# Performance work log

Measured on AMD Instinct MI355X. Metric: run time of the kernel, lower is better.

The kernel has to match this reference:

```python
import jax, jax.numpy as jnp
import numpy as np

N_NODES = 100000
N_EDGES = 3200000
F_IN = 256
F_OUT = 256


def setup_inputs() -> dict:
    key = jax.random.key(0)
    k1, k2, k3, k4, k5, k6 = jax.random.split(key, 6)
    x = jax.random.normal(k1, (N_NODES, F_IN), dtype=jnp.float32)
    edge_rows = jax.random.randint(k2, (N_EDGES,), 0, N_NODES, dtype=jnp.int64)
    edge_cols = jax.random.randint(k3, (N_EDGES,), 0, N_NODES, dtype=jnp.int64)
    edge_vals = jax.random.uniform(k4, (N_EDGES,), dtype=jnp.float32)
    weight = jax.random.normal(k5, (F_IN, F_OUT), dtype=jnp.float32) * (1.0 / np.sqrt(F_OUT))
    b = jax.random.normal(k6, (F_OUT,), dtype=jnp.float32) * (1.0 / np.sqrt(F_OUT))
    return {"x": x, "edge_rows": edge_rows, "edge_cols": edge_cols,
            "edge_vals": edge_vals, "weight": weight, "b": b}


def reference(x, edge_rows, edge_cols, edge_vals, weight, b):
    # support = X @ W  (dense GEMM)
    support = x @ weight  # (N, F_out)
    # SpMM: out[r] = sum_e vals[e] * support[cols[e]] for edges with rows[e]==r
    gathered = edge_vals[:, None] * support[edge_cols]  # (E, F_out)
    out = jax.ops.segment_sum(gathered, edge_rows, num_segments=N_NODES)
    return out + b
```

## Files before the change

### kernel.cpp

```cpp
#include <hip/hip_runtime.h>


#define SH 6
#define BROWS 64
#define CAPSLOT 2560
#define ACHUNK 16384
#define MAXNB 2048

using short8 = __attribute__((ext_vector_type(8))) short;
using f32x4  = __attribute__((ext_vector_type(4))) float;

__device__ __forceinline__ float bf2f(unsigned short h) {
  union { unsigned u; float f; } v; v.u = ((unsigned)h) << 16; return v.f;
}
__device__ __forceinline__ unsigned short f2bf(float f) {
  union { float f; unsigned u; } v; v.f = f;
  unsigned u = v.u;
  unsigned r = (u + 0x7FFFu + ((u >> 16) & 1u)) >> 16;
  return (unsigned short)r;
}

__global__ void k_conv_w(const float* __restrict__ W,
                         unsigned short* __restrict__ Whi,
                         unsigned short* __restrict__ Wlo) {
  int bx = blockIdx.x;
  int lane = threadIdx.x;
  int t = bx >> 3, s = bx & 7;
  int n  = t * 16 + (lane & 15);
  int k0 = s * 32 + (lane >> 4) * 8;
  unsigned short hh[8], ll[8];
#pragma unroll
  for (int j = 0; j < 8; ++j) {
    float w = W[(k0 + j) * 256 + n];
    unsigned short h = f2bf(w);
    hh[j] = h;
    ll[j] = f2bf(w - bf2f(h));
  }
  uint4 uh, ul;
  uh.x = (unsigned)hh[0] | ((unsigned)hh[1] << 16);
  uh.y = (unsigned)hh[2] | ((unsigned)hh[3] << 16);
  uh.z = (unsigned)hh[4] | ((unsigned)hh[5] << 16);
  uh.w = (unsigned)hh[6] | ((unsigned)hh[7] << 16);
  ul.x = (unsigned)ll[0] | ((unsigned)ll[1] << 16);
  ul.y = (unsigned)ll[2] | ((unsigned)ll[3] << 16);
  ul.z = (unsigned)ll[4] | ((unsigned)ll[5] << 16);
  ul.w = (unsigned)ll[6] | ((unsigned)ll[7] << 16);
  size_t o = ((size_t)bx * 64 + lane) * 8;
  *(uint4*)(Whi + o) = uh;
  *(uint4*)(Wlo + o) = ul;
}

__global__ __launch_bounds__(256) void k_gemm(const float* __restrict__ x,
                                              const unsigned short* __restrict__ Whi,
                                              const unsigned short* __restrict__ Wlo,
                                              unsigned short* __restrict__ sup,
                                              int n_nodes) {
  __shared__ alignas(16) unsigned short Ahi[8 * 512];
  __shared__ alignas(16) unsigned short Alo[8 * 512];
  const int m0 = blockIdx.x * 16;
  {
    int t = threadIdx.x;
    int row = t >> 4;
    int kbase = (t & 15) << 4;
    int s = kbase >> 5;
    int quad0 = (kbase >> 3) & 3;
    float v[16];
    int gr = m0 + row;
    if (gr < n_nodes) {
      const float4* px = (const float4*)(x + (size_t)gr * 256 + kbase);
#pragma unroll
      for (int q = 0; q < 4; ++q) {
        float4 f = px[q];
        v[q * 4 + 0] = f.x; v[q * 4 + 1] = f.y; v[q * 4 + 2] = f.z; v[q * 4 + 3] = f.w;
      }
    } else {
#pragma unroll
      for (int j = 0; j < 16; ++j) v[j] = 0.0f;
    }
    unsigned short h[16], l[16];
#pragma unroll
    for (int j = 0; j < 16; ++j) {
      unsigned short hb = f2bf(v[j]);
      h[j] = hb;
      l[j] = f2bf(v[j] - bf2f(hb));
    }
    uint4 u;
    u.x = (unsigned)h[0] | ((unsigned)h[1] << 16);
    u.y = (unsigned)h[2] | ((unsigned)h[3] << 16);
    u.z = (unsigned)h[4] | ((unsigned)h[5] << 16);
    u.w = (unsigned)h[6] | ((unsigned)h[7] << 16);
    *(uint4*)&Ahi[s * 512 + (quad0 * 16 + row) * 8] = u;
    u.x = (unsigned)h[8]  | ((unsigned)h[9]  << 16);
    u.y = (unsigned)h[10] | ((unsigned)h[11] << 16);
    u.z = (unsigned)h[12] | ((unsigned)h[13] << 16);
    u.w = (unsigned)h[14] | ((unsigned)h[15] << 16);
    *(uint4*)&Ahi[s * 512 + ((quad0 + 1) * 16 + row) * 8] = u;
    u.x = (unsigned)l[0] | ((unsigned)l[1] << 16);
    u.y = (unsigned)l[2] | ((unsigned)l[3] << 16);
    u.z = (unsigned)l[4] | ((unsigned)l[5] << 16);
    u.w = (unsigned)l[6] | ((unsigned)l[7] << 16);
    *(uint4*)&Alo[s * 512 + (quad0 * 16 + row) * 8] = u;
    u.x = (unsigned)l[8]  | ((unsigned)l[9]  << 16);
    u.y = (unsigned)l[10] | ((unsigned)l[11] << 16);
    u.z = (unsigned)l[12] | ((unsigned)l[13] << 16);
    u.w = (unsigned)l[14] | ((unsigned)l[15] << 16);
    *(uint4*)&Alo[s * 512 + ((quad0 + 1) * 16 + row) * 8] = u;
  }
  __syncthreads();
  const int lane = threadIdx.x & 63;
  const int wave = threadIdx.x >> 6;
  f32x4 acc0 = {0,0,0,0}, acc1 = {0,0,0,0}, acc2 = {0,0,0,0}, acc3 = {0,0,0,0};
  const short8* AH = (const short8*)Ahi;
  const short8* AL = (const short8*)Alo;
  const short8* BH = (const short8*)Whi;
  const short8* BL = (const short8*)Wlo;
  const int tn = wave * 4;
#pragma unroll
  for (int s = 0; s < 8; ++s) {
    short8 ah = AH[s * 64 + lane];
    short8 al = AL[s * 64 + lane];
    short8 bh0 = BH[((tn + 0) * 8 + s) * 64 + lane];
    short8 bh1 = BH[((tn + 1) * 8 + s) * 64 + lane];
    short8 bh2 = BH[((tn + 2) * 8 + s) * 64 + lane];
    short8 bh3 = BH[((tn + 3) * 8 + s) * 64 + lane];
    short8 bl0 = BL[((tn + 0) * 8 + s) * 64 + lane];
    short8 bl1 = BL[((tn + 1) * 8 + s) * 64 + lane];
    short8 bl2 = BL[((tn + 2) * 8 + s) * 64 + lane];
    short8 bl3 = BL[((tn + 3) * 8 + s) * 64 + lane];
    acc0 = __builtin_amdgcn_mfma_f32_16x16x32_bf16(ah, bh0, acc0, 0, 0, 0);
    acc1 = __builtin_amdgcn_mfma_f32_16x16x32_bf16(ah, bh1, acc1, 0, 0, 0);
    acc2 = __builtin_amdgcn_mfma_f32_16x16x32_bf16(ah, bh2, acc2, 0, 0, 0);
    acc3 = __builtin_amdgcn_mfma_f32_16x16x32_bf16(ah, bh3, acc3, 0, 0, 0);
    acc0 = __builtin_amdgcn_mfma_f32_16x16x32_bf16(ah, bl0, acc0, 0, 0, 0);
    acc1 = __builtin_amdgcn_mfma_f32_16x16x32_bf16(ah, bl1, acc1, 0, 0, 0);
    acc2 = __builtin_amdgcn_mfma_f32_16x16x32_bf16(ah, bl2, acc2, 0, 0, 0);
    acc3 = __builtin_amdgcn_mfma_f32_16x16x32_bf16(ah, bl3, acc3, 0, 0, 0);
    acc0 = __builtin_amdgcn_mfma_f32_16x16x32_bf16(al, bh0, acc0, 0, 0, 0);
    acc1 = __builtin_amdgcn_mfma_f32_16x16x32_bf16(al, bh1, acc1, 0, 0, 0);
    acc2 = __builtin_amdgcn_mfma_f32_16x16x32_bf16(al, bh2, acc2, 0, 0, 0);
    acc3 = __builtin_amdgcn_mfma_f32_16x16x32_bf16(al, bh3, acc3, 0, 0, 0);
  }
  const int quad = lane >> 4;
  const int col  = lane & 15;
  f32x4 accs[4] = {acc0, acc1, acc2, acc3};
#pragma unroll
  for (int i = 0; i < 4; ++i) {
    int n = (tn + i) * 16 + col;
#pragma unroll
    for (int r = 0; r < 4; ++r) {
      int m = m0 + quad * 4 + r;
      if (m < n_nodes) sup[(size_t)m * 256 + n] = f2bf(accs[i][r]);
    }
  }
}

__global__ __launch_bounds__(256) void k_bscatter(const int* __restrict__ rows,
                                                  const int* __restrict__ cols,
                                                  const float* __restrict__ vals,
                                                  unsigned* __restrict__ bucketCount,
                                                  uint2* __restrict__ cvA,
                                                  int E, int NB) {
  __shared__ unsigned h[MAXNB];
  __shared__ unsigned baseS[MAXNB];
  for (int i = threadIdx.x; i < NB; i += 256) h[i] = 0;
  __syncthreads();
  int base = blockIdx.x * ACHUNK;
  int lim = min(ACHUNK, E - base);
  for (int i = threadIdx.x; i < lim; i += 256)
    atomicAdd(&h[rows[base + i] >> SH], 1u);
  __syncthreads();
  for (int i = threadIdx.x; i < NB; i += 256) {
    unsigned c = h[i];
    baseS[i] = c ? ((unsigned)i * CAPSLOT + atomicAdd(&bucketCount[i], c)) : 0u;
  }
  __syncthreads();
  for (int i = threadIdx.x; i < NB; i += 256) h[i] = 0;
  __syncthreads();
  for (int i = threadIdx.x; i < lim; i += 256) {
    int e = base + i;
    int r = rows[e];
    int b = r >> SH;
    unsigned off = atomicAdd(&h[b], 1u);
    unsigned pos = baseS[b] + off;
    union { float f; unsigned u; } v; v.f = vals[e];
    unsigned key = (unsigned)cols[e] | ((unsigned)(r & (BROWS - 1)) << 17);
    cvA[pos] = make_uint2(key, v.u);
  }
}

__global__ __launch_bounds__(256) void k_bspmm(const unsigned* __restrict__ bucketCount,
                                               const uint2* __restrict__ cvA,
                                               const unsigned short* __restrict__ sup,
                                               const float* __restrict__ bias,
                                               float* __restrict__ out,
                                               int n_nodes) {
  __shared__ uint2 scv[CAPSLOT];
  __shared__ unsigned hist[BROWS];
  __shared__ unsigned startS[BROWS + 1];
  __shared__ unsigned cur[BROWS];
  const int b = blockIdx.x;
  const int tid = threadIdx.x;
  const unsigned beg = (unsigned)b * CAPSLOT;
  int cnt = (int)bucketCount[b];
  if (cnt > CAPSLOT) cnt = CAPSLOT;
  if (tid < BROWS) hist[tid] = 0;
  __syncthreads();
  for (int i = tid; i < cnt; i += 256)
    atomicAdd(&hist[cvA[beg + i].x >> 17], 1u);
  __syncthreads();
  if (tid == 0) {
    unsigned run = 0;
#pragma unroll
    for (int j = 0; j < BROWS; ++j) { startS[j] = run; run += hist[j]; }
    startS[BROWS] = run;
  }
  __syncthreads();
  if (tid < BROWS) cur[tid] = startS[tid];
  __syncthreads();
  for (int i = tid; i < cnt; i += 256) {
    uint2 c = cvA[beg + i];
    unsigned p = atomicAdd(&cur[c.x >> 17], 1u);
    scv[p] = c;
  }
  __syncthreads();
  const int wave = tid >> 6;
  const int lane = tid & 63;
  const unsigned short* supl = sup + lane * 4;
  float4 b4 = *(const float4*)(bias + lane * 4);
  for (int lr = wave; lr < BROWS; lr += 4) {
    int gr = (b << SH) + lr;
    if (gr >= n_nodes) break;
    float ax = b4.x, ay = b4.y, az = b4.z, aw = b4.w;
    unsigned e = startS[lr], t1 = startS[lr + 1];
    for (; e + 8 <= t1; e += 8) {
      uint2 c[8]; ushort4 g[8];
#pragma unroll
      for (int j = 0; j < 8; ++j) c[j] = scv[e + j];
#pragma unroll
      for (int j = 0; j < 8; ++j)
        g[j] = *(const ushort4*)(supl + (size_t)(c[j].x & 0x1FFFFu) * 256);
#pragma unroll
      for (int j = 0; j < 8; ++j) {
        union { unsigned u; float f; } v{c[j].y};
        ax = fmaf(v.f, bf2f(g[j].x), ax); ay = fmaf(v.f, bf2f(g[j].y), ay);
        az = fmaf(v.f, bf2f(g[j].z), az); aw = fmaf(v.f, bf2f(g[j].w), aw);
      }
    }
    for (; e + 4 <= t1; e += 4) {
      uint2 c[4]; ushort4 g[4];
#pragma unroll
      for (int j = 0; j < 4; ++j) c[j] = scv[e + j];
#pragma unroll
      for (int j = 0; j < 4; ++j)
        g[j] = *(const ushort4*)(supl + (size_t)(c[j].x & 0x1FFFFu) * 256);
#pragma unroll
      for (int j = 0; j < 4; ++j) {
        union { unsigned u; float f; } v{c[j].y};
        ax = fmaf(v.f, bf2f(g[j].x), ax); ay = fmaf(v.f, bf2f(g[j].y), ay);
        az = fmaf(v.f, bf2f(g[j].z), az); aw = fmaf(v.f, bf2f(g[j].w), aw);
      }
    }
    for (; e < t1; ++e) {
      uint2 c = scv[e];
      ushort4 g = *(const ushort4*)(supl + (size_t)(c.x & 0x1FFFFu) * 256);
      union { unsigned u; float f; } v{c.y};
      ax = fmaf(v.f, bf2f(g.x), ax); ay = fmaf(v.f, bf2f(g.y), ay);
      az = fmaf(v.f, bf2f(g.z), az); aw = fmaf(v.f, bf2f(g.w), aw);
    }
    float4 o; o.x = ax; o.y = ay; o.z = az; o.w = aw;
    *(float4*)(out + (size_t)gr * 256 + lane * 4) = o;
  }
}

extern "C" void kernel_launch(void* const* d_in, const int* in_sizes, int n_in,
                              void* d_out, int out_size, void* d_ws, size_t ws_size,
                              hipStream_t stream) {
  const float* x    = (const float*)d_in[0];
  const int*   rows = (const int*)d_in[1];
  const int*   cols = (const int*)d_in[2];
  const float* vals = (const float*)d_in[3];
  const float* W    = (const float*)d_in[4];
  const float* bias = (const float*)d_in[5];
  float* out = (float*)d_out;

  const int n_nodes = in_sizes[0] / 256;
  const int E       = in_sizes[1];
  const int NB      = (n_nodes + BROWS - 1) >> SH;
  (void)n_in; (void)out_size; (void)ws_size;

  char* ws = (char*)d_ws;
  size_t off = 0;
  auto alloc = [&](size_t bytes) { size_t o = off; off += (bytes + 255) & ~(size_t)255; return o; };
  unsigned short* Whi    = (unsigned short*)(ws + alloc(65536 * 2));
  unsigned short* Wlo    = (unsigned short*)(ws + alloc(65536 * 2));
  unsigned short* sup    = (unsigned short*)(ws + alloc((size_t)n_nodes * 256 * 2));
  unsigned* bucketCount  = (unsigned*)(ws + alloc((size_t)NB * 4));
  uint2* cvA             = (uint2*)(ws + alloc((size_t)NB * CAPSLOT * 8));

  const int nA = (E + ACHUNK - 1) / ACHUNK;

  hipMemsetAsync(bucketCount, 0, (size_t)NB * 4, stream);
  k_conv_w<<<128, 64, 0, stream>>>(W, Whi, Wlo);
  k_gemm<<<(n_nodes + 15) / 16, 256, 0, stream>>>(x, Whi, Wlo, sup, n_nodes);
  k_bscatter<<<nA, 256, 0, stream>>>(rows, cols, vals, bucketCount, cvA, E, NB);
  k_bspmm<<<NB, 256, 0, stream>>>(bucketCount, cvA, sup, bias, out, n_nodes);
}
```

Baseline: 621.7 us.

## Fuse GEMM and edge bucket scatter into one launch, halve bucket size

```diff
diff --git a/kernel.cpp b/kernel.cpp
--- a/kernel.cpp
+++ b/kernel.cpp
@@ -1,11 +1,11 @@
 #include <hip/hip_runtime.h>
 
 
-#define SH 6
-#define BROWS 64
-#define CAPSLOT 2560
-#define ACHUNK 16384
-#define MAXNB 2048
+#define SH 5
+#define BROWS 32
+#define CAPSLOT 1280
+#define ACHUNK 8192
+#define MAXNB 3200
 
 using short8 = __attribute__((ext_vector_type(8))) short;
 using f32x4  = __attribute__((ext_vector_type(4))) float;
@@ -50,14 +50,52 @@
   *(uint4*)(Wlo + o) = ul;
 }
 
-__global__ __launch_bounds__(256) void k_gemm(const float* __restrict__ x,
-                                              const unsigned short* __restrict__ Whi,
-                                              const unsigned short* __restrict__ Wlo,
-                                              unsigned short* __restrict__ sup,
-                                              int n_nodes) {
-  __shared__ alignas(16) unsigned short Ahi[8 * 512];
-  __shared__ alignas(16) unsigned short Alo[8 * 512];
-  const int m0 = blockIdx.x * 16;
+struct GemmSmem { alignas(16) unsigned short Ahi[8 * 512]; alignas(16) unsigned short Alo[8 * 512]; };
+struct ScatSmem { unsigned h[MAXNB]; };
+
+__global__ __launch_bounds__(256) void k_gemm_scatter(
+    const float* __restrict__ x,
+    const unsigned short* __restrict__ Whi,
+    const unsigned short* __restrict__ Wlo,
+    unsigned short* __restrict__ sup,
+    int n_nodes,
+    const int* __restrict__ rows,
+    const int* __restrict__ cols,
+    const float* __restrict__ vals,
+    unsigned* __restrict__ bucketCount,
+    uint2* __restrict__ cvA,
+    int E, int NB, int nScat) {
+  __shared__ union { GemmSmem g; ScatSmem s; } sm;
+
+  if ((int)blockIdx.x < nScat) {
+    unsigned* h = sm.s.h;
+    int base = (int)blockIdx.x * ACHUNK;
+    int lim = min(ACHUNK, E - base);
+    for (int i = threadIdx.x; i < NB; i += 256) h[i] = 0u;
+    __syncthreads();
+    for (int i = threadIdx.x; i < lim; i += 256)
+      atomicAdd(&h[rows[base + i] >> SH], 1u);
+    __syncthreads();
+    for (int i = threadIdx.x; i < NB; i += 256) {
+      unsigned c = h[i];
+      if (c) h[i] = (unsigned)i * CAPSLOT + atomicAdd(&bucketCount[i], c);
+    }
+    __syncthreads();
+    for (int i = threadIdx.x; i < lim; i += 256) {
+      int e = base + i;
+      int r = rows[e];
+      unsigned pos = atomicAdd(&h[r >> SH], 1u);
+      union { float f; unsigned u; } v;
+      v.f = __builtin_nontemporal_load(vals + e);
+      unsigned key = (unsigned)__builtin_nontemporal_load(cols + e) |
+                     ((unsigned)(r & (BROWS - 1)) << 17);
+      unsigned long long pk = (unsigned long long)key | ((unsigned long long)v.u << 32);
+      __builtin_nontemporal_store(pk, (unsigned long long*)&cvA[pos]);
+    }
+    return;
+  }
+
+  const int m0 = ((int)blockIdx.x - nScat) * 16;
   {
     int t = threadIdx.x;
     int row = t >> 4;
@@ -67,11 +105,11 @@
     float v[16];
     int gr = m0 + row;
     if (gr < n_nodes) {
-      const float4* px = (const float4*)(x + (size_t)gr * 256 + kbase);
+      const f32x4* px = (const f32x4*)(x + (size_t)gr * 256 + kbase);
 #pragma unroll
       for (int q = 0; q < 4; ++q) {
-        float4 f = px[q];
-        v[q * 4 + 0] = f.x; v[q * 4 + 1] = f.y; v[q * 4 + 2] = f.z; v[q * 4 + 3] = f.w;
+        f32x4 f = __builtin_nontemporal_load(px + q);
+        v[q * 4 + 0] = f[0]; v[q * 4 + 1] = f[1]; v[q * 4 + 2] = f[2]; v[q * 4 + 3] = f[3];
       }
     } else {
 #pragma unroll
@@ -89,29 +127,29 @@
     u.y = (unsigned)h[2] | ((unsigned)h[3] << 16);
     u.z = (unsigned)h[4] | ((unsigned)h[5] << 16);
     u.w = (unsigned)h[6] | ((unsigned)h[7] << 16);
-    *(uint4*)&Ahi[s * 512 + (quad0 * 16 + row) * 8] = u;
+    *(uint4*)&sm.g.Ahi[s * 512 + (quad0 * 16 + row) * 8] = u;
     u.x = (unsigned)h[8]  | ((unsigned)h[9]  << 16);
     u.y = (unsigned)h[10] | ((unsigned)h[11] << 16);
     u.z = (unsigned)h[12] | ((unsigned)h[13] << 16);
     u.w = (unsigned)h[14] | ((unsigned)h[15] << 16);
-    *(uint4*)&Ahi[s * 512 + ((quad0 + 1) * 16 + row) * 8] = u;
+    *(uint4*)&sm.g.Ahi[s * 512 + ((quad0 + 1) * 16 + row) * 8] = u;
     u.x = (unsigned)l[0] | ((unsigned)l[1] << 16);
     u.y = (unsigned)l[2] | ((unsigned)l[3] << 16);
     u.z = (unsigned)l[4] | ((unsigned)l[5] << 16);
     u.w = (unsigned)l[6] | ((unsigned)l[7] << 16);
-    *(uint4*)&Alo[s * 512 + (quad0 * 16 + row) * 8] = u;
+    *(uint4*)&sm.g.Alo[s * 512 + (quad0 * 16 + row) * 8] = u;
     u.x = (unsigned)l[8]  | ((unsigned)l[9]  << 16);
     u.y = (unsigned)l[10] | ((unsigned)l[11] << 16);
     u.z = (unsigned)l[12] | ((unsigned)l[13] << 16);
     u.w = (unsigned)l[14] | ((unsigned)l[15] << 16);
-    *(uint4*)&Alo[s * 512 + ((quad0 + 1) * 16 + row) * 8] = u;
+    *(uint4*)&sm.g.Alo[s * 512 + ((quad0 + 1) * 16 + row) * 8] = u;
   }
   __syncthreads();
   const int lane = threadIdx.x & 63;
   const int wave = threadIdx.x >> 6;
   f32x4 acc0 = {0,0,0,0}, acc1 = {0,0,0,0}, acc2 = {0,0,0,0}, acc3 = {0,0,0,0};
-  const short8* AH = (const short8*)Ahi;
-  const short8* AL = (const short8*)Alo;
+  const short8* AH = (const short8*)sm.g.Ahi;
+  const short8* AL = (const short8*)sm.g.Alo;
   const short8* BH = (const short8*)Whi;
   const short8* BL = (const short8*)Wlo;
   const int tn = wave * 4;
@@ -154,40 +192,6 @@
   }
 }
 
-__global__ __launch_bounds__(256) void k_bscatter(const int* __restrict__ rows,
-                                                  const int* __restrict__ cols,
-                                                  const float* __restrict__ vals,
-                                                  unsigned* __restrict__ bucketCount,
-                                                  uint2* __restrict__ cvA,
-                                                  int E, int NB) {
-  __shared__ unsigned h[MAXNB];
-  __shared__ unsigned baseS[MAXNB];
-  for (int i = threadIdx.x; i < NB; i += 256) h[i] = 0;
-  __syncthreads();
-  int base = blockIdx.x * ACHUNK;
-  int lim = min(ACHUNK, E - base);
-  for (int i = threadIdx.x; i < lim; i += 256)
-    atomicAdd(&h[rows[base + i] >> SH], 1u);
-  __syncthreads();
-  for (int i = threadIdx.x; i < NB; i += 256) {
-    unsigned c = h[i];
-    baseS[i] = c ? ((unsigned)i * CAPSLOT + atomicAdd(&bucketCount[i], c)) : 0u;
-  }
-  __syncthreads();
-  for (int i = threadIdx.x; i < NB; i += 256) h[i] = 0;
-  __syncthreads();
-  for (int i = threadIdx.x; i < lim; i += 256) {
-    int e = base + i;
-    int r = rows[e];
-    int b = r >> SH;
-    unsigned off = atomicAdd(&h[b], 1u);
-    unsigned pos = baseS[b] + off;
-    union { float f; unsigned u; } v; v.f = vals[e];
-    unsigned key = (unsigned)cols[e] | ((unsigned)(r & (BROWS - 1)) << 17);
-    cvA[pos] = make_uint2(key, v.u);
-  }
-}
-
 __global__ __launch_bounds__(256) void k_bspmm(const unsigned* __restrict__ bucketCount,
                                                const uint2* __restrict__ cvA,
                                                const unsigned short* __restrict__ sup,
@@ -226,11 +230,11 @@
   const int wave = tid >> 6;
   const int lane = tid & 63;
   const unsigned short* supl = sup + lane * 4;
-  float4 b4 = *(const float4*)(bias + lane * 4);
+  f32x4 b4 = *(const f32x4*)(bias + lane * 4);
   for (int lr = wave; lr < BROWS; lr += 4) {
     int gr = (b << SH) + lr;
     if (gr >= n_nodes) break;
-    float ax = b4.x, ay = b4.y, az = b4.z, aw = b4.w;
+    float ax = b4[0], ay = b4[1], az = b4[2], aw = b4[3];
     unsigned e = startS[lr], t1 = startS[lr + 1];
     for (; e + 8 <= t1; e += 8) {
       uint2 c[8]; ushort4 g[8];
@@ -267,8 +271,8 @@
       ax = fmaf(v.f, bf2f(g.x), ax); ay = fmaf(v.f, bf2f(g.y), ay);
       az = fmaf(v.f, bf2f(g.z), az); aw = fmaf(v.f, bf2f(g.w), aw);
     }
-    float4 o; o.x = ax; o.y = ay; o.z = az; o.w = aw;
-    *(float4*)(out + (size_t)gr * 256 + lane * 4) = o;
+    f32x4 o; o[0] = ax; o[1] = ay; o[2] = az; o[3] = aw;
+    __builtin_nontemporal_store(o, (f32x4*)(out + (size_t)gr * 256 + lane * 4));
   }
 }
 
@@ -297,11 +301,13 @@
   unsigned* bucketCount  = (unsigned*)(ws + alloc((size_t)NB * 4));
   uint2* cvA             = (uint2*)(ws + alloc((size_t)NB * CAPSLOT * 8));
 
-  const int nA = (E + ACHUNK - 1) / ACHUNK;
+  const int nScat = (E + ACHUNK - 1) / ACHUNK;
+  const int nGemm = (n_nodes + 15) / 16;
 
   hipMemsetAsync(bucketCount, 0, (size_t)NB * 4, stream);
   k_conv_w<<<128, 64, 0, stream>>>(W, Whi, Wlo);
-  k_gemm<<<(n_nodes + 15) / 16, 256, 0, stream>>>(x, Whi, Wlo, sup, n_nodes);
-  k_bscatter<<<nA, 256, 0, stream>>>(rows, cols, vals, bucketCount, cvA, E, NB);
+  k_gemm_scatter<<<nScat + nGemm, 256, 0, stream>>>(x, Whi, Wlo, sup, n_nodes,
+                                                    rows, cols, vals,
+                                                    bucketCount, cvA, E, NB, nScat);
   k_bspmm<<<NB, 256, 0, stream>>>(bucketCount, cvA, sup, bias, out, n_nodes);
 }
```

After: 603.7 us. -2.9%, faster.
